# Optimization experiments

Measured on AMD Instinct MI355X. Metric: run time of the kernel, lower is better.

The kernel has to match this reference:

```python
import jax, jax.numpy as jnp
import numpy as np

B, L, D = 8, 2048, 64

def setup_inputs() -> dict:
    key = jax.random.key(0)
    k1, k2 = jax.random.split(key)
    query = jax.random.normal(k1, (B, L, D), dtype=jnp.float32)
    key_t = jax.random.normal(k2, (B, L, D), dtype=jnp.float32)
    return {"query": query, "key": key_t}

def reference(query, key):
    d = query.shape[-1]
    # scores: [B, Lq, Lk] = Q K^T / sqrt(d)
    scores = jnp.einsum('bqd,bkd->bqk', query, key) / jnp.sqrt(jnp.asarray(d, query.dtype))
    weights = jax.nn.softmax(scores, axis=-1)  # dropout p=0.0 -> identity
    # output uses `key` as values, matching the original module
    return jnp.einsum('bqk,bkd->bqd', weights, key)
```

## Files before the change

### kernel.cpp

```cpp
#include <hip/hip_runtime.h>
#include <hip/hip_bf16.h>


#define LL 2048
#define DD 64
#define BQ 128
#define BK 64
#define KPAD 72
#define NSEG 8

typedef __attribute__((ext_vector_type(8))) short bf16x8;
typedef __attribute__((ext_vector_type(4))) float f32x4;
typedef __attribute__((ext_vector_type(4))) unsigned short u16x4;

static __device__ __forceinline__ unsigned short f2bf(float f) {
  unsigned u = __builtin_bit_cast(unsigned, f);
  u += 0x7fffu + ((u >> 16) & 1u);
  return (unsigned short)(u >> 16);
}
static __device__ __forceinline__ float bf2f(unsigned short h) {
  unsigned u = (unsigned)h << 16;
  return __builtin_bit_cast(float, u);
}

__global__ __launch_bounds__(256, 4) void attn_kernel(
    const float* __restrict__ Q, const float* __restrict__ K,
    float* __restrict__ O, unsigned short* __restrict__ Opart,
    float* __restrict__ Lp, int seglen, int nseg) {
  __shared__ __attribute__((aligned(16))) unsigned short sKt[BK][KPAD];
  __shared__ __attribute__((aligned(16))) unsigned short sKtT[DD * KPAD];
  __shared__ __attribute__((aligned(16))) unsigned short sP[4][32][KPAD];

  const int tid  = threadIdx.x;
  const int wave = tid >> 6;
  const int lane = tid & 63;
  const int quad = lane >> 4;
  const int l16  = lane & 15;

  const int batch = blockIdx.y;
  const int seg   = blockIdx.z;
  const int q0w   = blockIdx.x * BQ + wave * 32;
  const int BLrows = gridDim.y * LL;

  const float qs = 0.125f * 1.44269504f;
  bf16x8 bq[2][2];
#pragma unroll
  for (int qt = 0; qt < 2; ++qt) {
    const float* qrow = Q + (size_t)(batch * LL + q0w + qt * 16 + l16) * DD;
#pragma unroll
    for (int ks = 0; ks < 2; ++ks) {
      const float* p = qrow + ks * 32 + quad * 8;
      float4 f0 = *(const float4*)(p);
      float4 f1 = *(const float4*)(p + 4);
      bf16x8 a;
      a[0] = (short)f2bf(f0.x * qs); a[1] = (short)f2bf(f0.y * qs);
      a[2] = (short)f2bf(f0.z * qs); a[3] = (short)f2bf(f0.w * qs);
      a[4] = (short)f2bf(f1.x * qs); a[5] = (short)f2bf(f1.y * qs);
      a[6] = (short)f2bf(f1.z * qs); a[7] = (short)f2bf(f1.w * qs);
      bq[qt][ks] = a;
    }
  }

  f32x4 oacc[2][4];
  float l_part[2];
#pragma unroll
  for (int qt = 0; qt < 2; ++qt) {
#pragma unroll
    for (int n = 0; n < 4; ++n) oacc[qt][n] = (f32x4){0.f, 0.f, 0.f, 0.f};
    l_part[qt] = 0.f;
  }

  const int niter = seglen / BK;
  const float4* kseg = (const float4*)(K + (size_t)(batch * LL + seg * seglen) * DD);

  float4 pf[2][2];
#pragma unroll
  for (int i = 0; i < 2; ++i) {
    int p = tid + i * 256;
    pf[i][0] = kseg[p * 2];
    pf[i][1] = kseg[p * 2 + 1];
  }

  for (int t = 0; t < niter; ++t) {
    __syncthreads();

#pragma unroll
    for (int i = 0; i < 2; ++i) {
      int p  = tid + i * 256;
      int kv = p >> 3;
      int oc = p & 7;
      unsigned short h[8];
      h[0] = f2bf(pf[i][0].x); h[1] = f2bf(pf[i][0].y);
      h[2] = f2bf(pf[i][0].z); h[3] = f2bf(pf[i][0].w);
      h[4] = f2bf(pf[i][1].x); h[5] = f2bf(pf[i][1].y);
      h[6] = f2bf(pf[i][1].z); h[7] = f2bf(pf[i][1].w);
      *(bf16x8*)&sKt[kv][oc * 8] = *(const bf16x8*)h;
      int swz = (((kv >> 3) ^ oc) & 7) * 8 + (kv & 7);
      unsigned short* dst = &sKtT[(oc * 8) * KPAD + swz];
#pragma unroll
      for (int j = 0; j < 8; ++j) dst[j * KPAD] = h[j];
    }

    if (t + 1 < niter) {
      const float4* ksrc = kseg + (t + 1) * (BK * DD / 4);
#pragma unroll
      for (int i = 0; i < 2; ++i) {
        int p = tid + i * 256;
        pf[i][0] = ksrc[p * 2];
        pf[i][1] = ksrc[p * 2 + 1];
      }
    }
    __syncthreads();

    f32x4 s[2][4];
#pragma unroll
    for (int mt = 0; mt < 4; ++mt) {
      bf16x8 k0 = *(const bf16x8*)&sKt[mt * 16 + l16][quad * 8];
      bf16x8 k1 = *(const bf16x8*)&sKt[mt * 16 + l16][32 + quad * 8];
      f32x4 z = (f32x4){0.f, 0.f, 0.f, 0.f};
      s[0][mt] = __builtin_amdgcn_mfma_f32_16x16x32_bf16(k0, bq[0][0], z, 0, 0, 0);
      s[0][mt] = __builtin_amdgcn_mfma_f32_16x16x32_bf16(k1, bq[0][1], s[0][mt], 0, 0, 0);
      s[1][mt] = __builtin_amdgcn_mfma_f32_16x16x32_bf16(k0, bq[1][0], z, 0, 0, 0);
      s[1][mt] = __builtin_amdgcn_mfma_f32_16x16x32_bf16(k1, bq[1][1], s[1][mt], 0, 0, 0);
    }

#pragma unroll
    for (int qt = 0; qt < 2; ++qt) {
#pragma unroll
      for (int mt = 0; mt < 4; ++mt) {
        u16x4 h;
#pragma unroll
        for (int r = 0; r < 4; ++r) {
          float p = __builtin_amdgcn_exp2f(s[qt][mt][r]);
          l_part[qt] += p;
          h[r] = f2bf(p);
        }
        *(u16x4*)&sP[wave][qt * 16 + l16][mt * 16 + quad * 4] = h;
      }
    }

#pragma unroll
    for (int ks = 0; ks < 2; ++ks) {
      bf16x8 a0 = *(const bf16x8*)&sP[wave][l16][ks * 32 + quad * 8];
      bf16x8 a1 = *(const bf16x8*)&sP[wave][16 + l16][ks * 32 + quad * 8];
#pragma unroll
      for (int nt = 0; nt < 4; ++nt) {
        int d = nt * 16 + l16;
        bf16x8 b = *(const bf16x8*)&sKtT[d * KPAD + (((ks * 4 + quad) ^ (d >> 3)) & 7) * 8];
        oacc[0][nt] = __builtin_amdgcn_mfma_f32_16x16x32_bf16(a0, b, oacc[0][nt], 0, 0, 0);
        oacc[1][nt] = __builtin_amdgcn_mfma_f32_16x16x32_bf16(a1, b, oacc[1][nt], 0, 0, 0);
      }
    }
  }

#pragma unroll
  for (int qt = 0; qt < 2; ++qt) {
    l_part[qt] += __shfl_xor(l_part[qt], 16);
    l_part[qt] += __shfl_xor(l_part[qt], 32);
  }

  if (nseg == 1) {
#pragma unroll
    for (int qt = 0; qt < 2; ++qt)
#pragma unroll
      for (int r = 0; r < 4; ++r) {
        float lr = __shfl(l_part[qt], (lane & 48) | (quad * 4 + r), 64);
        float invl = 1.0f / lr;
        float* orow = O + (size_t)(batch * LL + q0w + qt * 16 + quad * 4 + r) * DD;
#pragma unroll
        for (int nt = 0; nt < 4; ++nt)
          orow[nt * 16 + l16] = oacc[qt][nt][r] * invl;
      }
  } else {
#pragma unroll
    for (int qt = 0; qt < 2; ++qt) {
      if (quad == 0)
        Lp[seg * BLrows + batch * LL + q0w + qt * 16 + l16] = l_part[qt];
#pragma unroll
      for (int r = 0; r < 4; ++r) {
        int row = batch * LL + q0w + qt * 16 + quad * 4 + r;
        unsigned short* op = Opart + ((size_t)seg * BLrows + row) * DD;
#pragma unroll
        for (int nt = 0; nt < 4; ++nt)
          op[nt * 16 + l16] = f2bf(oacc[qt][nt][r]);
      }
    }
  }
}

__global__ __launch_bounds__(256) void combine_kernel(
    const unsigned short* __restrict__ Opart, const float* __restrict__ Lp,
    float* __restrict__ O, int nseg, int BLrows) {
  const int tid = threadIdx.x;
  const int row = blockIdx.x * 4 + (tid >> 6);
  const int d   = tid & 63;
  float denom = 0.f, acc = 0.f;
  for (int s = 0; s < nseg; ++s) {
    denom += Lp[s * BLrows + row];
    acc   += bf2f(Opart[((size_t)s * BLrows + row) * DD + d]);
  }
  O[(size_t)row * DD + d] = acc / denom;
}

extern "C" void kernel_launch(void* const* d_in, const int* in_sizes, int n_in,
                              void* d_out, int out_size, void* d_ws, size_t ws_size,
                              hipStream_t stream) {
  const float* Q = (const float*)d_in[0];
  const float* K = (const float*)d_in[1];
  float* O = (float*)d_out;
  int B = in_sizes[0] / (LL * DD);
  int BLrows = B * LL;

  size_t need = (size_t)NSEG * BLrows * DD * sizeof(unsigned short) +
                (size_t)NSEG * BLrows * sizeof(float);
  if (ws_size >= need) {
    unsigned short* Opart = (unsigned short*)d_ws;
    float* Lpp = (float*)(Opart + (size_t)NSEG * BLrows * DD);
    dim3 grid(LL / BQ, B, NSEG);
    attn_kernel<<<grid, 256, 0, stream>>>(Q, K, O, Opart, Lpp, LL / NSEG, NSEG);
    combine_kernel<<<dim3(BLrows / 4), 256, 0, stream>>>(Opart, Lpp, O, NSEG, BLrows);
  } else {
    dim3 grid(LL / BQ, B, 1);
    attn_kernel<<<grid, 256, 0, stream>>>(Q, K, O, nullptr, nullptr, LL, 1);
  }
}
```

Baseline: 92.29 us.

## Load K fragments directly from global for QK, drop register prefetch, fragment-native partials

Removes the row-major K tile from LDS and has each wave load its QK MFMA operands straight from global memory (L2/L1), converting to bf16 in registers. The register double-buffer prefetch of the next K tile is dropped, so the transposed K tile is loaded and written synchronously each iteration. Partial outputs are now stored in MFMA fragment order as packed 4-wide bf16 vectors and the combine kernel reads that layout, so writes and reads are wide and coalesced. This trades LDS traffic and capacity for redundant global loads per wave and loses load/compute overlap.

```diff
diff --git a/kernel.cpp b/kernel.cpp
--- a/kernel.cpp
+++ b/kernel.cpp
@@ -8,6 +8,7 @@
 #define BK 64
 #define KPAD 72
 #define NSEG 8
+#define NQB (LL / BQ)
 
 typedef __attribute__((ext_vector_type(8))) short bf16x8;
 typedef __attribute__((ext_vector_type(4))) float f32x4;
@@ -25,9 +26,8 @@
 
 __global__ __launch_bounds__(256, 4) void attn_kernel(
     const float* __restrict__ Q, const float* __restrict__ K,
-    float* __restrict__ O, unsigned short* __restrict__ Opart,
+    float* __restrict__ O, u16x4* __restrict__ Opart,
     float* __restrict__ Lp, int seglen, int nseg) {
-  __shared__ __attribute__((aligned(16))) unsigned short sKt[BK][KPAD];
   __shared__ __attribute__((aligned(16))) unsigned short sKtT[DD * KPAD];
   __shared__ __attribute__((aligned(16))) unsigned short sP[4][32][KPAD];
 
@@ -40,7 +40,8 @@
   const int batch = blockIdx.y;
   const int seg   = blockIdx.z;
   const int q0w   = blockIdx.x * BQ + wave * 32;
-  const int BLrows = gridDim.y * LL;
+  const int ngroups = gridDim.y * NQB;
+  const int gq    = batch * NQB + blockIdx.x;
 
   const float qs = 0.125f * 1.44269504f;
   bf16x8 bq[2][2];
@@ -71,15 +72,7 @@
   }
 
   const int niter = seglen / BK;
-  const float4* kseg = (const float4*)(K + (size_t)(batch * LL + seg * seglen) * DD);
-
-  float4 pf[2][2];
-#pragma unroll
-  for (int i = 0; i < 2; ++i) {
-    int p = tid + i * 256;
-    pf[i][0] = kseg[p * 2];
-    pf[i][1] = kseg[p * 2 + 1];
-  }
+  const float* kbase = K + (size_t)(batch * LL + seg * seglen) * DD;
 
   for (int t = 0; t < niter; ++t) {
     __syncthreads();
@@ -89,34 +82,36 @@
       int p  = tid + i * 256;
       int kv = p >> 3;
       int oc = p & 7;
+      const float4* src = (const float4*)(kbase + (size_t)(t * BK + kv) * DD + oc * 8);
+      float4 f0 = src[0];
+      float4 f1 = src[1];
       unsigned short h[8];
-      h[0] = f2bf(pf[i][0].x); h[1] = f2bf(pf[i][0].y);
-      h[2] = f2bf(pf[i][0].z); h[3] = f2bf(pf[i][0].w);
-      h[4] = f2bf(pf[i][1].x); h[5] = f2bf(pf[i][1].y);
-      h[6] = f2bf(pf[i][1].z); h[7] = f2bf(pf[i][1].w);
-      *(bf16x8*)&sKt[kv][oc * 8] = *(const bf16x8*)h;
-      int swz = (((kv >> 3) ^ oc) & 7) * 8 + (kv & 7);
-      unsigned short* dst = &sKtT[(oc * 8) * KPAD + swz];
+      h[0] = f2bf(f0.x); h[1] = f2bf(f0.y); h[2] = f2bf(f0.z); h[3] = f2bf(f0.w);
+      h[4] = f2bf(f1.x); h[5] = f2bf(f1.y); h[6] = f2bf(f1.z); h[7] = f2bf(f1.w);
+      int swz = ((kv >> 3) ^ oc) & 7;
+      unsigned short* dst = &sKtT[(oc * 8) * KPAD + swz * 8 + (kv & 7)];
 #pragma unroll
       for (int j = 0; j < 8; ++j) dst[j * KPAD] = h[j];
     }
-
-    if (t + 1 < niter) {
-      const float4* ksrc = kseg + (t + 1) * (BK * DD / 4);
-#pragma unroll
-      for (int i = 0; i < 2; ++i) {
-        int p = tid + i * 256;
-        pf[i][0] = ksrc[p * 2];
-        pf[i][1] = ksrc[p * 2 + 1];
-      }
-    }
     __syncthreads();
 
     f32x4 s[2][4];
 #pragma unroll
     for (int mt = 0; mt < 4; ++mt) {
-      bf16x8 k0 = *(const bf16x8*)&sKt[mt * 16 + l16][quad * 8];
-      bf16x8 k1 = *(const bf16x8*)&sKt[mt * 16 + l16][32 + quad * 8];
+      const float* ar = kbase + (size_t)(t * BK + mt * 16 + l16) * DD + quad * 8;
+      float4 a00 = *(const float4*)(ar);
+      float4 a01 = *(const float4*)(ar + 4);
+      float4 a10 = *(const float4*)(ar + 32);
+      float4 a11 = *(const float4*)(ar + 36);
+      bf16x8 k0, k1;
+      k0[0] = (short)f2bf(a00.x); k0[1] = (short)f2bf(a00.y);
+      k0[2] = (short)f2bf(a00.z); k0[3] = (short)f2bf(a00.w);
+      k0[4] = (short)f2bf(a01.x); k0[5] = (short)f2bf(a01.y);
+      k0[6] = (short)f2bf(a01.z); k0[7] = (short)f2bf(a01.w);
+      k1[0] = (short)f2bf(a10.x); k1[1] = (short)f2bf(a10.y);
+      k1[2] = (short)f2bf(a10.z); k1[3] = (short)f2bf(a10.w);
+      k1[4] = (short)f2bf(a11.x); k1[5] = (short)f2bf(a11.y);
+      k1[6] = (short)f2bf(a11.z); k1[7] = (short)f2bf(a11.w);
       f32x4 z = (f32x4){0.f, 0.f, 0.f, 0.f};
       s[0][mt] = __builtin_amdgcn_mfma_f32_16x16x32_bf16(k0, bq[0][0], z, 0, 0, 0);
       s[0][mt] = __builtin_amdgcn_mfma_f32_16x16x32_bf16(k1, bq[0][1], s[0][mt], 0, 0, 0);
@@ -171,35 +166,50 @@
         for (int nt = 0; nt < 4; ++nt)
           orow[nt * 16 + l16] = oacc[qt][nt][r] * invl;
       }
-  } else {
-#pragma unroll
-    for (int qt = 0; qt < 2; ++qt) {
-      if (quad == 0)
-        Lp[seg * BLrows + batch * LL + q0w + qt * 16 + l16] = l_part[qt];
-#pragma unroll
-      for (int r = 0; r < 4; ++r) {
-        int row = batch * LL + q0w + qt * 16 + quad * 4 + r;
-        unsigned short* op = Opart + ((size_t)seg * BLrows + row) * DD;
-#pragma unroll
-        for (int nt = 0; nt < 4; ++nt)
-          op[nt * 16 + l16] = f2bf(oacc[qt][nt][r]);
-      }
-    }
+    return;
+  }
+
+  const size_t slotbase = ((size_t)seg * ngroups + gq) * 32 + wave * 8;
+#pragma unroll
+  for (int qt = 0; qt < 2; ++qt) {
+#pragma unroll
+    for (int nt = 0; nt < 4; ++nt) {
+      u16x4 h;
+      h[0] = f2bf(oacc[qt][nt][0]); h[1] = f2bf(oacc[qt][nt][1]);
+      h[2] = f2bf(oacc[qt][nt][2]); h[3] = f2bf(oacc[qt][nt][3]);
+      Opart[(slotbase + qt * 4 + nt) * 64 + lane] = h;
+    }
+    if (quad == 0)
+      Lp[(((size_t)seg * ngroups + gq) * 8 + wave * 2 + qt) * 16 + l16] = l_part[qt];
   }
 }
 
 __global__ __launch_bounds__(256) void combine_kernel(
-    const unsigned short* __restrict__ Opart, const float* __restrict__ Lp,
-    float* __restrict__ O, int nseg, int BLrows) {
-  const int tid = threadIdx.x;
-  const int row = blockIdx.x * 4 + (tid >> 6);
-  const int d   = tid & 63;
-  float denom = 0.f, acc = 0.f;
+    const u16x4* __restrict__ Opart, const float* __restrict__ Lp,
+    float* __restrict__ O, int nseg, int ngroups) {
+  const int tid  = threadIdx.x;
+  const int g    = blockIdx.x;
+  const int slot = blockIdx.y * 4 + (tid >> 6);
+  const int lane = tid & 63;
+  const int quad = lane >> 4;
+  const int l16  = lane & 15;
+  const int wv = slot >> 3, qt = (slot >> 2) & 1, nt = slot & 3;
+
+  f32x4 acc = (f32x4){0.f, 0.f, 0.f, 0.f};
+  float den = 0.f;
   for (int s = 0; s < nseg; ++s) {
-    denom += Lp[s * BLrows + row];
-    acc   += bf2f(Opart[((size_t)s * BLrows + row) * DD + d]);
-  }
-  O[(size_t)row * DD + d] = acc / denom;
+    u16x4 h = Opart[((size_t)(s * ngroups + g) * 32 + slot) * 64 + lane];
+    acc[0] += bf2f(h[0]); acc[1] += bf2f(h[1]);
+    acc[2] += bf2f(h[2]); acc[3] += bf2f(h[3]);
+    den += Lp[((size_t)(s * ngroups + g) * 8 + wv * 2 + qt) * 16 + l16];
+  }
+  const int batch = g / NQB, qbx = g % NQB;
+  const int rowbase = batch * LL + qbx * BQ + wv * 32 + qt * 16;
+#pragma unroll
+  for (int r = 0; r < 4; ++r) {
+    float dr = __shfl(den, (lane & 48) | (quad * 4 + r), 64);
+    O[(size_t)(rowbase + quad * 4 + r) * DD + nt * 16 + l16] = acc[r] / dr;
+  }
 }
 
 extern "C" void kernel_launch(void* const* d_in, const int* in_sizes, int n_in,
@@ -209,18 +219,18 @@
   const float* K = (const float*)d_in[1];
   float* O = (float*)d_out;
   int B = in_sizes[0] / (LL * DD);
-  int BLrows = B * LL;
-
-  size_t need = (size_t)NSEG * BLrows * DD * sizeof(unsigned short) +
-                (size_t)NSEG * BLrows * sizeof(float);
-  if (ws_size >= need) {
-    unsigned short* Opart = (unsigned short*)d_ws;
-    float* Lpp = (float*)(Opart + (size_t)NSEG * BLrows * DD);
-    dim3 grid(LL / BQ, B, NSEG);
+  int ngroups = B * NQB;
+
+  size_t opart_bytes = (size_t)NSEG * ngroups * 32 * 64 * sizeof(u16x4);
+  size_t lp_bytes    = (size_t)NSEG * ngroups * 8 * 16 * sizeof(float);
+  if (ws_size >= opart_bytes + lp_bytes) {
+    u16x4* Opart = (u16x4*)d_ws;
+    float* Lpp = (float*)((char*)d_ws + opart_bytes);
+    dim3 grid(NQB, B, NSEG);
     attn_kernel<<<grid, 256, 0, stream>>>(Q, K, O, Opart, Lpp, LL / NSEG, NSEG);
-    combine_kernel<<<dim3(BLrows / 4), 256, 0, stream>>>(Opart, Lpp, O, NSEG, BLrows);
+    combine_kernel<<<dim3(ngroups, 8), 256, 0, stream>>>(Opart, Lpp, O, NSEG, ngroups);
   } else {
-    dim3 grid(LL / BQ, B, 1);
+    dim3 grid(NQB, B, 1);
     attn_kernel<<<grid, 256, 0, stream>>>(Q, K, O, nullptr, nullptr, LL, 1);
   }
 }
```

Result: slower. 105.0 us (+13.8%).
